# Optimization experiments

Hardware: AMD Instinct MI355X
Metric: run time of the kernel (lower is better)

The kernel has to match this reference:

```python
import jax, jax.numpy as jnp
import numpy as np

B, T, DIM = 4, 2048, 512
HEADS, HD = 8, 64
RANK = 256
WIN = 256
EPS = 1e-6
ROPE_BASE = 10000.0


def _rope_tables(seq_len, head_dim):
    pos = jnp.arange(seq_len, dtype=jnp.float32)                      # [T]
    inv_freq = 1.0 / (ROPE_BASE ** (jnp.arange(0, head_dim, 2, dtype=jnp.float32) / head_dim))  # [HD/2]
    ang = pos[:, None] * inv_freq[None, :]                            # [T, HD/2]
    cos = jnp.concatenate([jnp.cos(ang), jnp.cos(ang)], axis=-1)      # [T, HD]
    sin = jnp.concatenate([jnp.sin(ang), jnp.sin(ang)], axis=-1)
    return cos, sin


def _rotate_half(x):
    x1, x2 = jnp.split(x, 2, axis=-1)
    return jnp.concatenate([-x2, x1], axis=-1)


def _apply_rope(q, k):
    # q, k: [B, H, T, HD]
    cos, sin = _rope_tables(q.shape[2], q.shape[3])
    cos = cos[None, None]; sin = sin[None, None]
    q = q * cos + _rotate_half(q) * sin
    k = k * cos + _rotate_half(k) * sin
    return q, k


def _rmsnorm(x, w):
    x32 = x.astype(jnp.float32)
    n = x32 * jax.lax.rsqrt(jnp.mean(x32 * x32, axis=-1, keepdims=True) + EPS)
    return n.astype(x.dtype) * w


def setup_inputs() -> dict:
    key = jax.random.key(0)
    ks = jax.random.split(key, 6)
    s = 0.02
    return {
        "x": jax.random.normal(ks[0], (B, T, DIM), dtype=jnp.float32),
        "Wq": jax.random.normal(ks[1], (DIM, DIM), dtype=jnp.float32) * s,
        "Wkv_down": jax.random.normal(ks[2], (RANK, DIM), dtype=jnp.float32) * s,
        "kv_norm_w": jnp.ones((RANK,), dtype=jnp.float32),
        "Wkv_up": jax.random.normal(ks[3], (2 * DIM, RANK), dtype=jnp.float32) * s,
        "Wout": jax.random.normal(ks[4], (DIM, DIM), dtype=jnp.float32) * s,
    }


def reference(x, Wq, Wkv_down, kv_norm_w, Wkv_up, Wout):
    # q projection -> [B, H, T, HD]
    q = jnp.einsum('btd,ed->bte', x, Wq).reshape(B, T, HEADS, HD).transpose(0, 2, 1, 3)
    # latent KV: down-proj -> RMSNorm -> up-proj
    c_kv = jnp.einsum('btd,rd->btr', x, Wkv_down)          # [B, T, RANK]
    c_kv = _rmsnorm(c_kv, kv_norm_w)
    kv = jnp.einsum('btr,er->bte', c_kv, Wkv_up)            # [B, T, 2*DIM]
    kv = kv.reshape(B, T, 2, HEADS, HD).transpose(2, 0, 3, 1, 4)
    k, v = kv[0], kv[1]                                     # [B, H, T, HD]
    q, k = _apply_rope(q, k)
    rows = jnp.arange(T)[:, None]
    cols = jnp.arange(T)[None, :]
    mask = jnp.abs(cols - rows) <= WIN                      # [T, T]
    scale = HD ** -0.5
    scores = jnp.einsum('bhtd,bhsd->bhts', q, k) * scale    # [B, H, T, T]
    scores = jnp.where(mask[None, None], scores, jnp.float32(-jnp.inf))
    attn = jax.nn.softmax(scores, axis=-1)
    out = jnp.einsum('bhts,bhsd->bhtd', attn, v)            # [B, H, T, HD]
    out = out.transpose(0, 2, 1, 3).reshape(B, T, DIM)
    return jnp.einsum('btd,ed->bte', out, Wout)
```

## Files before the change

kernel.cpp:

```cpp
#include <hip/hip_runtime.h>
#include <math.h>

#define BB 4
#define TT 2048
#define DIMM 512
#define HEADS 8
#define HDIM 64
#define RANKK 256
#define WINN 256

static constexpr int BT = BB * TT;
#define SC2 0.1803368801111244f

typedef short bf8_t __attribute__((ext_vector_type(8)));
typedef float f32x4 __attribute__((ext_vector_type(4)));

__device__ __forceinline__ unsigned short f2bf(float f) {
    unsigned u = __float_as_uint(f);
    u += 0x7fffu + ((u >> 16) & 1u);
    return (unsigned short)(u >> 16);
}
__device__ __forceinline__ unsigned f2bf2(float a, float b) {
    unsigned r;
    asm("v_cvt_pk_bf16_f32 %0, %1, %2" : "=v"(r) : "v"(a), "v"(b));
    return r;
}

typedef __attribute__((address_space(1))) void gvoid_t;
typedef __attribute__((address_space(3))) void lvoid_t;
__device__ __forceinline__ void gload16(const void* g, void* l) {
    __builtin_amdgcn_global_load_lds((gvoid_t*)g, (lvoid_t*)l, 16, 0, 0);
}
#define WAIT_VM0_BARRIER() do { \
    asm volatile("s_waitcnt vmcnt(0)" ::: "memory"); \
    __builtin_amdgcn_s_barrier(); \
    __builtin_amdgcn_sched_barrier(0); \
} while (0)

__device__ __forceinline__ void cvt4(const float* __restrict__ s,
                                     unsigned short* __restrict__ d, int i) {
    float4 v = *reinterpret_cast<const float4*>(s + i);
    uint2 st = make_uint2(f2bf2(v.x, v.y), f2bf2(v.z, v.w));
    *reinterpret_cast<uint2*>(d + i) = st;
}

__global__ __launch_bounds__(256) void prep_kernel(
    const float* __restrict__ x, const float* __restrict__ Wq,
    const float* __restrict__ Wkd, const float* __restrict__ Wku,
    const float* __restrict__ wn, const float* __restrict__ Wout,
    unsigned short* __restrict__ xb, unsigned short* __restrict__ wcomb,
    unsigned short* __restrict__ wkub, unsigned short* __restrict__ woutb,
    float* __restrict__ cosT, float* __restrict__ sinT) {
    int bid = blockIdx.x;
    if (bid < 4096) {
        cvt4(x, xb, (bid * 256 + threadIdx.x) * 4);
    } else if (bid < 4352) {
        cvt4(Wq, wcomb, ((bid - 4096) * 256 + threadIdx.x) * 4);
    } else if (bid < 4480) {
        cvt4(Wkd, wcomb + DIMM * DIMM, ((bid - 4352) * 256 + threadIdx.x) * 4);
    } else if (bid < 4736) {
        int i = ((bid - 4480) * 256 + threadIdx.x) * 4;
        float4 v = *reinterpret_cast<const float4*>(Wku + i);
        float4 s = *reinterpret_cast<const float4*>(wn + (i & 255));
        uint2 st = make_uint2(f2bf2(v.x * s.x, v.y * s.y), f2bf2(v.z * s.z, v.w * s.w));
        *reinterpret_cast<uint2*>(wkub + i) = st;
    } else if (bid < 4992) {
        cvt4(Wout, woutb, ((bid - 4736) * 256 + threadIdx.x) * 4);
    } else {
        int idx = (bid - 4992) * 256 + threadIdx.x;
        int t = idx >> 5, f = idx & 31;
        double freq = pow(10000.0, -(double)f / 32.0);
        double ang = (double)t * freq;
        cosT[idx] = (float)cos(ang);
        sinT[idx] = (float)sin(ang);
    }
}

template<int MODE, int BM>
__global__ __launch_bounds__(BM * 4) void gemm_bf(const unsigned short* __restrict__ A,
                                                  const unsigned short* __restrict__ W,
                                                  float* __restrict__ Cf,
                                                  unsigned short* __restrict__ O1,
                                                  unsigned short* __restrict__ O2,
                                                  const float* __restrict__ cosT,
                                                  const float* __restrict__ sinT,
                                                  float* __restrict__ ssum,
                                                  int K, int N) {
    __shared__ __align__(16) unsigned short As[2][BM * 64];
    __shared__ __align__(16) unsigned short Ws[2][128 * 64];
    const int tid = threadIdx.x;
    const int lane = tid & 63, w = tid >> 6;
    const int lr = lane & 15, hi = lane >> 4;
    const int m0 = blockIdx.x * BM, n0 = blockIdx.y * 128;
    const int wr = (w >> 1) * 32, wc = (w & 1) * 64;

    f32x4 acc[2][4];
#pragma unroll
    for (int i = 0; i < 2; ++i)
#pragma unroll
        for (int j = 0; j < 4; ++j) acc[i][j] = 0.0f;

    const int NT = K >> 6;
    auto stage = [&](int t, int b) {
        const int kt = t * 64;
#pragma unroll
        for (int c = tid; c < BM * 8; c += BM * 4) {
            int row = c >> 3, sc = ((c & 7) ^ (row & 7)) << 3;
            gload16(A + (size_t)(m0 + row) * K + kt + sc, &As[b][c * 8]);
        }
#pragma unroll
        for (int c = tid; c < 1024; c += BM * 4) {
            int row = c >> 3, sc = ((c & 7) ^ (row & 7)) << 3;
            gload16(W + (size_t)(n0 + row) * K + kt + sc, &Ws[b][c * 8]);
        }
    };

    stage(0, 0);
    WAIT_VM0_BARRIER();
    for (int t = 0; t < NT; ++t) {
        const int cur = t & 1;
        if (t + 1 < NT) stage(t + 1, cur ^ 1);
        bf8_t af[2][2], bw[4][2];
#pragma unroll
        for (int i = 0; i < 2; ++i) {
            int row = wr + i * 16 + lr;
#pragma unroll
            for (int kk = 0; kk < 2; ++kk)
                af[i][kk] = *reinterpret_cast<const bf8_t*>(
                    &As[cur][row * 64 + (((kk * 4 + hi) ^ (row & 7)) << 3)]);
        }
#pragma unroll
        for (int j = 0; j < 4; ++j) {
            int row = wc + j * 16 + lr;
#pragma unroll
            for (int kk = 0; kk < 2; ++kk)
                bw[j][kk] = *reinterpret_cast<const bf8_t*>(
                    &Ws[cur][row * 64 + (((kk * 4 + hi) ^ (row & 7)) << 3)]);
        }
#pragma unroll
        for (int kk = 0; kk < 2; ++kk)
#pragma unroll
            for (int i = 0; i < 2; ++i)
#pragma unroll
                for (int j = 0; j < 4; ++j)
                    acc[i][j] = __builtin_amdgcn_mfma_f32_16x16x32_bf16(af[i][kk], bw[j][kk], acc[i][j], 0, 0, 0);
        if (t + 1 < NT) WAIT_VM0_BARRIER();
    }

    if constexpr (MODE == 0) {
#pragma unroll
        for (int i = 0; i < 2; ++i)
#pragma unroll
            for (int j = 0; j < 4; ++j)
#pragma unroll
                for (int r = 0; r < 4; ++r)
                    Cf[(size_t)(m0 + wr + i * 16 + 4 * hi + r) * N + n0 + wc + j * 16 + lr] = acc[i][j][r];
    } else if (n0 < 512) {
        int h = (n0 + wc) >> 6;
#pragma unroll
        for (int i = 0; i < 2; ++i) {
            int tb = m0 + wr + i * 16 + 4 * hi;
            float4 rv4 = make_float4(1.f, 1.f, 1.f, 1.f);
            if constexpr (MODE == 2) {
                float4 sa = *reinterpret_cast<const float4*>(ssum + tb);
                float4 sb = *reinterpret_cast<const float4*>(ssum + 8192 + tb);
                float4 sc = *reinterpret_cast<const float4*>(ssum + 16384 + tb);
                float4 sd = *reinterpret_cast<const float4*>(ssum + 24576 + tb);
                rv4.x = rsqrtf((sa.x + sb.x + sc.x + sd.x) * (1.0f / RANKK) + 1e-6f);
                rv4.y = rsqrtf((sa.y + sb.y + sc.y + sd.y) * (1.0f / RANKK) + 1e-6f);
                rv4.z = rsqrtf((sa.z + sb.z + sc.z + sd.z) * (1.0f / RANKK) + 1e-6f);
                rv4.w = rsqrtf((sa.w + sb.w + sc.w + sd.w) * (1.0f / RANKK) + 1e-6f);
            }
#pragma unroll
            for (int j = 0; j < 2; ++j)
#pragma unroll
                for (int r = 0; r < 4; ++r) {
                    int t = tb + r;
                    int b = t >> 11, tt = t & 2047;
                    int ff = j * 16 + lr;
                    float rv = (&rv4.x)[r];
                    float x1 = acc[i][j][r] * rv, x2 = acc[i][j + 2][r] * rv;
                    float cc = cosT[tt * 32 + ff], ss = sinT[tt * 32 + ff];
                    unsigned u = f2bf2(x1 * cc - x2 * ss, x2 * cc + x1 * ss);
                    unsigned short* dp = O1 + ((size_t)((b * 8 + h) * 2048 + tt)) * 64;
                    dp[ff]      = (unsigned short)u;
                    dp[ff + 32] = (unsigned short)(u >> 16);
                }
        }
    } else if constexpr (MODE == 1) {
        int cb = n0 - 512 + wc;
        int part = ((n0 - 512) >> 7) * 2 + (w & 1);
#pragma unroll
        for (int i = 0; i < 2; ++i) {
            int tb = m0 + wr + i * 16 + 4 * hi;
#pragma unroll
            for (int r = 0; r < 4; ++r) {
                float ps = acc[i][0][r] * acc[i][0][r] + acc[i][1][r] * acc[i][1][r]
                         + acc[i][2][r] * acc[i][2][r] + acc[i][3][r] * acc[i][3][r];
                ps += __shfl_xor(ps, 1);
                ps += __shfl_xor(ps, 2);
                ps += __shfl_xor(ps, 4);
                ps += __shfl_xor(ps, 8);
                if (lr == 0) ssum[part * 8192 + tb + r] = ps;
            }
#pragma unroll
            for (int j = 0; j < 4; ++j) {
                unsigned a01 = f2bf2(acc[i][j][0], acc[i][j][1]);
                unsigned a23 = f2bf2(acc[i][j][2], acc[i][j][3]);
                unsigned short* dp = O2 + (size_t)tb * 256 + cb + j * 16 + lr;
                dp[0]   = (unsigned short)a01;
                dp[256] = (unsigned short)(a01 >> 16);
                dp[512] = (unsigned short)a23;
                dp[768] = (unsigned short)(a23 >> 16);
            }
        }
    } else {
        int cb = n0 + wc - 512;
        int h = cb >> 6;
#pragma unroll
        for (int i = 0; i < 2; ++i) {
            int tb = m0 + wr + i * 16 + 4 * hi;
            int b = tb >> 11, tt = tb & 2047;
            float4 sa = *reinterpret_cast<const float4*>(ssum + tb);
            float4 sb = *reinterpret_cast<const float4*>(ssum + 8192 + tb);
            float4 sc = *reinterpret_cast<const float4*>(ssum + 16384 + tb);
            float4 sd = *reinterpret_cast<const float4*>(ssum + 24576 + tb);
            float4 rv4;
            rv4.x = rsqrtf((sa.x + sb.x + sc.x + sd.x) * (1.0f / RANKK) + 1e-6f);
            rv4.y = rsqrtf((sa.y + sb.y + sc.y + sd.y) * (1.0f / RANKK) + 1e-6f);
            rv4.z = rsqrtf((sa.z + sb.z + sc.z + sd.z) * (1.0f / RANKK) + 1e-6f);
            rv4.w = rsqrtf((sa.w + sb.w + sc.w + sd.w) * (1.0f / RANKK) + 1e-6f);
#pragma unroll
            for (int j = 0; j < 4; ++j) {
                int hd = j * 16 + lr;
                uint2 st = make_uint2(f2bf2(acc[i][j][0] * rv4.x, acc[i][j][1] * rv4.y),
                                      f2bf2(acc[i][j][2] * rv4.z, acc[i][j][3] * rv4.w));
                *reinterpret_cast<uint2*>(O2 + (((size_t)(b * 8 + h) * 64 + hd) * 2048 + tt)) = st;
            }
        }
    }
}

__global__ __launch_bounds__(256) void attn_mfma(const unsigned short* __restrict__ qbf,
                                                 const unsigned short* __restrict__ kbf,
                                                 const unsigned short* __restrict__ vT,
                                                 unsigned short* __restrict__ aob) {
    __shared__ __align__(16) unsigned short Kl[2][64 * 64];
    __shared__ __align__(16) unsigned short Vl[2][64 * 64];
    __shared__ unsigned short Pl[128][72];
    const int tid = threadIdx.x;
    const int lane = tid & 63, w = tid >> 6;
    const int lr = lane & 15, hi = lane >> 4;

    const int fid = blockIdx.x;
    const int swz = (fid & 7) * 64 + (fid >> 3);
    const int t0 = (swz & 15) * 128;
    const int bh = swz >> 4;

    bf8_t qa[2][2];
#pragma unroll
    for (int qr = 0; qr < 2; ++qr) {
        const unsigned short* qp = qbf + ((size_t)bh * TT + t0 + w * 32 + qr * 16 + lr) * HDIM;
        qa[qr][0] = *reinterpret_cast<const bf8_t*>(qp + hi * 8);
        qa[qr][1] = *reinterpret_cast<const bf8_t*>(qp + 32 + hi * 8);
    }

    f32x4 oc[2][4];
#pragma unroll
    for (int qr = 0; qr < 2; ++qr)
#pragma unroll
        for (int f = 0; f < 4; ++f) oc[qr][f] = 0.0f;
    float lp[2][4] = {{0.f, 0.f, 0.f, 0.f}, {0.f, 0.f, 0.f, 0.f}};

    const int smin = max(0, t0 - WINN);
    const int smax = min(TT, t0 + 128 + WINN);
    const int NT = (smax - smin) >> 6;

    auto stage = [&](int t, int b) {
        const int s0 = smin + t * 64;
        int c0 = tid, c1 = tid + 256;
        int row0 = c0 >> 3, sc0 = ((c0 & 7) ^ (row0 & 7)) << 3;
        int row1 = c1 >> 3, sc1 = ((c1 & 7) ^ (row1 & 7)) << 3;
        gload16(kbf + ((size_t)bh * TT + s0 + row0) * HDIM + sc0, &Kl[b][c0 * 8]);
        gload16(kbf + ((size_t)bh * TT + s0 + row1) * HDIM + sc1, &Kl[b][c1 * 8]);
        gload16(vT + ((size_t)bh * 64 + row0) * TT + s0 + sc0, &Vl[b][c0 * 8]);
        gload16(vT + ((size_t)bh * 64 + row1) * TT + s0 + sc1, &Vl[b][c1 * 8]);
    };

    stage(0, 0);
    WAIT_VM0_BARRIER();
    for (int t = 0; t < NT; ++t) {
        const int cur = t & 1;
        if (t + 1 < NT) stage(t + 1, cur ^ 1);
        const int s0 = smin + t * 64;

        f32x4 sacc[2][4];
#pragma unroll
        for (int qr = 0; qr < 2; ++qr)
#pragma unroll
            for (int f = 0; f < 4; ++f) sacc[qr][f] = 0.0f;
        __builtin_amdgcn_s_setprio(1);
#pragma unroll
        for (int ks = 0; ks < 2; ++ks)
#pragma unroll
            for (int f = 0; f < 4; ++f) {
                int row = f * 16 + lr;
                bf8_t kb = *reinterpret_cast<const bf8_t*>(
                    &Kl[cur][row * 64 + (((ks * 4 + hi) ^ (row & 7)) << 3)]);
#pragma unroll
                for (int qr = 0; qr < 2; ++qr)
                    sacc[qr][f] = __builtin_amdgcn_mfma_f32_16x16x32_bf16(qa[qr][ks], kb, sacc[qr][f], 0, 0, 0);
            }
        __builtin_amdgcn_s_setprio(0);

        const int off_w = s0 - t0 - w * 32;
        const bool edge = (off_w + 63 > WINN) || (off_w - 31 < -WINN);
#pragma unroll
        for (int qr = 0; qr < 2; ++qr)
#pragma unroll
            for (int f = 0; f < 4; ++f) {
                float p[4];
#pragma unroll
                for (int r = 0; r < 4; ++r) {
                    float v;
                    if (edge) {
                        int d = off_w + f * 16 + lr - qr * 16 - 4 * hi - r;
                        v = (d <= WINN && d >= -WINN) ? exp2f(sacc[qr][f][r] * SC2) : 0.f;
                    } else {
                        v = exp2f(sacc[qr][f][r] * SC2);
                    }
                    p[r] = v;
                    lp[qr][r] += v;
                }
                unsigned a01 = f2bf2(p[0], p[1]);
                unsigned a23 = f2bf2(p[2], p[3]);
                unsigned short* bp = &Pl[w * 32 + qr * 16 + 4 * hi][f * 16 + lr];
                bp[0]   = (unsigned short)a01;
                bp[72]  = (unsigned short)(a01 >> 16);
                bp[144] = (unsigned short)a23;
                bp[216] = (unsigned short)(a23 >> 16);
            }

        __builtin_amdgcn_s_setprio(1);
#pragma unroll
        for (int ks = 0; ks < 2; ++ks) {
            bf8_t pa[2];
#pragma unroll
            for (int qr = 0; qr < 2; ++qr)
                pa[qr] = *reinterpret_cast<const bf8_t*>(&Pl[w * 32 + qr * 16 + lr][ks * 32 + hi * 8]);
#pragma unroll
            for (int f = 0; f < 4; ++f) {
                int row = f * 16 + lr;
                bf8_t vb = *reinterpret_cast<const bf8_t*>(
                    &Vl[cur][row * 64 + (((ks * 4 + hi) ^ (row & 7)) << 3)]);
#pragma unroll
                for (int qr = 0; qr < 2; ++qr)
                    oc[qr][f] = __builtin_amdgcn_mfma_f32_16x16x32_bf16(pa[qr], vb, oc[qr][f], 0, 0, 0);
            }
        }
        __builtin_amdgcn_s_setprio(0);
        if (t + 1 < NT) WAIT_VM0_BARRIER();
    }

#pragma unroll
    for (int qr = 0; qr < 2; ++qr)
#pragma unroll
        for (int r = 0; r < 4; ++r) {
            lp[qr][r] += __shfl_xor(lp[qr][r], 1);
            lp[qr][r] += __shfl_xor(lp[qr][r], 2);
            lp[qr][r] += __shfl_xor(lp[qr][r], 4);
            lp[qr][r] += __shfl_xor(lp[qr][r], 8);
        }

    int b = bh >> 3, h = bh & 7;
#pragma unroll
    for (int qr = 0; qr < 2; ++qr)
#pragma unroll
        for (int r = 0; r < 4; ++r) {
            float inv = 1.0f / lp[qr][r];
            int t = t0 + w * 32 + qr * 16 + 4 * hi + r;
            unsigned short* op = aob + ((size_t)b * TT + t) * DIMM + h * HDIM;
            unsigned u0 = f2bf2(oc[qr][0][r] * inv, oc[qr][1][r] * inv);
            unsigned u1 = f2bf2(oc[qr][2][r] * inv, oc[qr][3][r] * inv);
            op[lr]      = (unsigned short)u0;
            op[16 + lr] = (unsigned short)(u0 >> 16);
            op[32 + lr] = (unsigned short)u1;
            op[48 + lr] = (unsigned short)(u1 >> 16);
        }
}

extern "C" void kernel_launch(void* const* d_in, const int* in_sizes, int n_in,
                              void* d_out, int out_size, void* d_ws, size_t ws_size,
                              hipStream_t stream) {
    const float* x     = (const float*)d_in[0];
    const float* Wq    = (const float*)d_in[1];
    const float* Wkd   = (const float*)d_in[2];
    const float* wnorm = (const float*)d_in[3];
    const float* Wku   = (const float*)d_in[4];
    const float* Wout  = (const float*)d_in[5];
    float* out = (float*)d_out;
    char* ws = (char*)d_ws;

    unsigned short* xb    = (unsigned short*)(ws + 0);
    unsigned short* qb    = (unsigned short*)(ws + 8388608);
    unsigned short* kb    = (unsigned short*)(ws + 16777216);
    unsigned short* vTb   = (unsigned short*)(ws + 25165824);
    unsigned short* ckvb0 = (unsigned short*)(ws + 33554432);
    unsigned short* aob   = (unsigned short*)(ws + 37748736);
    unsigned short* wcomb = (unsigned short*)(ws + 46137344);
    unsigned short* wkub  = (unsigned short*)(ws + 46923776);
    unsigned short* woutb = (unsigned short*)(ws + 47448064);
    float*          cosT  = (float*)(ws + 48005120);
    float*          sinT  = (float*)(ws + 48267264);
    float*          ssum  = (float*)(ws + 48529408);

    prep_kernel<<<5248, 256, 0, stream>>>(x, Wq, Wkd, Wku, wnorm, Wout,
                                          xb, wcomb, wkub, woutb, cosT, sinT);

    gemm_bf<1, 64><<<dim3(BT / 64, 6), 256, 0, stream>>>(xb, wcomb, nullptr, qb, ckvb0,
                                                         cosT, sinT, ssum, DIMM, 768);

    gemm_bf<2, 128><<<dim3(BT / 128, 8), 512, 0, stream>>>(ckvb0, wkub, nullptr, kb, vTb,
                                                           cosT, sinT, ssum, RANKK, 1024);

    attn_mfma<<<512, 256, 0, stream>>>(qb, kb, vTb, aob);

    gemm_bf<0, 64><<<dim3(BT / 64, 4), 256, 0, stream>>>(aob, woutb, out, nullptr, nullptr,
                                                         nullptr, nullptr, nullptr, DIMM, DIMM);
}
```

Before: 81.19 us.

## Enlarge attention query tile to 256 rows with per-wave tile skipping, retile QKV GEMM

```diff
diff --git a/kernel.cpp b/kernel.cpp
--- a/kernel.cpp
+++ b/kernel.cpp
@@ -15,11 +15,6 @@
 typedef short bf8_t __attribute__((ext_vector_type(8)));
 typedef float f32x4 __attribute__((ext_vector_type(4)));
 
-__device__ __forceinline__ unsigned short f2bf(float f) {
-    unsigned u = __float_as_uint(f);
-    u += 0x7fffu + ((u >> 16) & 1u);
-    return (unsigned short)(u >> 16);
-}
 __device__ __forceinline__ unsigned f2bf2(float a, float b) {
     unsigned r;
     asm("v_cvt_pk_bf16_f32 %0, %1, %2" : "=v"(r) : "v"(a), "v"(b));
@@ -69,10 +64,11 @@
     } else {
         int idx = (bid - 4992) * 256 + threadIdx.x;
         int t = idx >> 5, f = idx & 31;
-        double freq = pow(10000.0, -(double)f / 32.0);
-        double ang = (double)t * freq;
-        cosT[idx] = (float)cos(ang);
-        sinT[idx] = (float)sin(ang);
+        double frev = exp2(-(double)f * 0.4152410118609203) * 0.15915494309189535;
+        double a = (double)t * frev;
+        float fr = (float)(a - floor(a));
+        cosT[idx] = cospif(2.0f * fr);
+        sinT[idx] = sinpif(2.0f * fr);
     }
 }
 
@@ -241,26 +237,27 @@
     }
 }
 
-__global__ __launch_bounds__(256) void attn_mfma(const unsigned short* __restrict__ qbf,
+__global__ __launch_bounds__(512) void attn_mfma(const unsigned short* __restrict__ qbf,
                                                  const unsigned short* __restrict__ kbf,
                                                  const unsigned short* __restrict__ vT,
                                                  unsigned short* __restrict__ aob) {
     __shared__ __align__(16) unsigned short Kl[2][64 * 64];
     __shared__ __align__(16) unsigned short Vl[2][64 * 64];
-    __shared__ unsigned short Pl[128][72];
+    __shared__ unsigned short Pl[256][72];
     const int tid = threadIdx.x;
     const int lane = tid & 63, w = tid >> 6;
     const int lr = lane & 15, hi = lane >> 4;
 
     const int fid = blockIdx.x;
-    const int swz = (fid & 7) * 64 + (fid >> 3);
-    const int t0 = (swz & 15) * 128;
-    const int bh = swz >> 4;
+    const int swz = (fid & 7) * 32 + (fid >> 3);
+    const int t0 = (swz & 7) * 256;
+    const int bh = swz >> 3;
+    const int wq0 = w * 32;
 
     bf8_t qa[2][2];
 #pragma unroll
     for (int qr = 0; qr < 2; ++qr) {
-        const unsigned short* qp = qbf + ((size_t)bh * TT + t0 + w * 32 + qr * 16 + lr) * HDIM;
+        const unsigned short* qp = qbf + ((size_t)bh * TT + t0 + wq0 + qr * 16 + lr) * HDIM;
         qa[qr][0] = *reinterpret_cast<const bf8_t*>(qp + hi * 8);
         qa[qr][1] = *reinterpret_cast<const bf8_t*>(qp + 32 + hi * 8);
     }
@@ -273,18 +270,16 @@
     float lp[2][4] = {{0.f, 0.f, 0.f, 0.f}, {0.f, 0.f, 0.f, 0.f}};
 
     const int smin = max(0, t0 - WINN);
-    const int smax = min(TT, t0 + 128 + WINN);
+    const int smax = min(TT, t0 + 256 + WINN);
     const int NT = (smax - smin) >> 6;
+
+    const int st_row = tid >> 3;
+    const int st_cs = ((tid & 7) ^ (st_row & 7)) << 3;
 
     auto stage = [&](int t, int b) {
         const int s0 = smin + t * 64;
-        int c0 = tid, c1 = tid + 256;
-        int row0 = c0 >> 3, sc0 = ((c0 & 7) ^ (row0 & 7)) << 3;
-        int row1 = c1 >> 3, sc1 = ((c1 & 7) ^ (row1 & 7)) << 3;
-        gload16(kbf + ((size_t)bh * TT + s0 + row0) * HDIM + sc0, &Kl[b][c0 * 8]);
-        gload16(kbf + ((size_t)bh * TT + s0 + row1) * HDIM + sc1, &Kl[b][c1 * 8]);
-        gload16(vT + ((size_t)bh * 64 + row0) * TT + s0 + sc0, &Vl[b][c0 * 8]);
-        gload16(vT + ((size_t)bh * 64 + row1) * TT + s0 + sc1, &Vl[b][c1 * 8]);
+        gload16(kbf + ((size_t)bh * TT + s0 + st_row) * HDIM + st_cs, &Kl[b][tid * 8]);
+        gload16(vT + ((size_t)bh * 64 + st_row) * TT + s0 + st_cs, &Vl[b][tid * 8]);
     };
 
     stage(0, 0);
@@ -293,72 +288,75 @@
         const int cur = t & 1;
         if (t + 1 < NT) stage(t + 1, cur ^ 1);
         const int s0 = smin + t * 64;
-
-        f32x4 sacc[2][4];
-#pragma unroll
-        for (int qr = 0; qr < 2; ++qr)
-#pragma unroll
-            for (int f = 0; f < 4; ++f) sacc[qr][f] = 0.0f;
-        __builtin_amdgcn_s_setprio(1);
-#pragma unroll
-        for (int ks = 0; ks < 2; ++ks)
-#pragma unroll
-            for (int f = 0; f < 4; ++f) {
-                int row = f * 16 + lr;
-                bf8_t kb = *reinterpret_cast<const bf8_t*>(
-                    &Kl[cur][row * 64 + (((ks * 4 + hi) ^ (row & 7)) << 3)]);
+        const int off_w = s0 - t0 - wq0;
+        const bool active = (off_w >= -(WINN + 63)) && (off_w <= WINN + 31);
+
+        if (active) {
+            f32x4 sacc[2][4];
+#pragma unroll
+            for (int qr = 0; qr < 2; ++qr)
+#pragma unroll
+                for (int f = 0; f < 4; ++f) sacc[qr][f] = 0.0f;
+            __builtin_amdgcn_s_setprio(1);
+#pragma unroll
+            for (int ks = 0; ks < 2; ++ks)
+#pragma unroll
+                for (int f = 0; f < 4; ++f) {
+                    int row = f * 16 + lr;
+                    bf8_t kb = *reinterpret_cast<const bf8_t*>(
+                        &Kl[cur][row * 64 + (((ks * 4 + hi) ^ (row & 7)) << 3)]);
+#pragma unroll
+                    for (int qr = 0; qr < 2; ++qr)
+                        sacc[qr][f] = __builtin_amdgcn_mfma_f32_16x16x32_bf16(qa[qr][ks], kb, sacc[qr][f], 0, 0, 0);
+                }
+            __builtin_amdgcn_s_setprio(0);
+
+            const bool edge = (off_w + 63 > WINN) || (off_w - 31 < -WINN);
+#pragma unroll
+            for (int qr = 0; qr < 2; ++qr)
+#pragma unroll
+                for (int f = 0; f < 4; ++f) {
+                    float p[4];
+#pragma unroll
+                    for (int r = 0; r < 4; ++r) {
+                        float v;
+                        if (edge) {
+                            int d = off_w + f * 16 + lr - qr * 16 - 4 * hi - r;
+                            v = (d <= WINN && d >= -WINN) ? exp2f(sacc[qr][f][r] * SC2) : 0.f;
+                        } else {
+                            v = exp2f(sacc[qr][f][r] * SC2);
+                        }
+                        p[r] = v;
+                        lp[qr][r] += v;
+                    }
+                    unsigned a01 = f2bf2(p[0], p[1]);
+                    unsigned a23 = f2bf2(p[2], p[3]);
+                    unsigned short* bp = &Pl[wq0 + qr * 16 + 4 * hi][f * 16 + lr];
+                    bp[0]   = (unsigned short)a01;
+                    bp[72]  = (unsigned short)(a01 >> 16);
+                    bp[144] = (unsigned short)a23;
+                    bp[216] = (unsigned short)(a23 >> 16);
+                }
+
+            __builtin_amdgcn_s_setprio(1);
+#pragma unroll
+            for (int ks = 0; ks < 2; ++ks) {
+                bf8_t pa[2];
 #pragma unroll
                 for (int qr = 0; qr < 2; ++qr)
-                    sacc[qr][f] = __builtin_amdgcn_mfma_f32_16x16x32_bf16(qa[qr][ks], kb, sacc[qr][f], 0, 0, 0);
+                    pa[qr] = *reinterpret_cast<const bf8_t*>(&Pl[wq0 + qr * 16 + lr][ks * 32 + hi * 8]);
+#pragma unroll
+                for (int f = 0; f < 4; ++f) {
+                    int row = f * 16 + lr;
+                    bf8_t vb = *reinterpret_cast<const bf8_t*>(
+                        &Vl[cur][row * 64 + (((ks * 4 + hi) ^ (row & 7)) << 3)]);
+#pragma unroll
+                    for (int qr = 0; qr < 2; ++qr)
+                        oc[qr][f] = __builtin_amdgcn_mfma_f32_16x16x32_bf16(pa[qr], vb, oc[qr][f], 0, 0, 0);
+                }
             }
-        __builtin_amdgcn_s_setprio(0);
-
-        const int off_w = s0 - t0 - w * 32;
-        const bool edge = (off_w + 63 > WINN) || (off_w - 31 < -WINN);
-#pragma unroll
-        for (int qr = 0; qr < 2; ++qr)
-#pragma unroll
-            for (int f = 0; f < 4; ++f) {
-                float p[4];
-#pragma unroll
-                for (int r = 0; r < 4; ++r) {
-                    float v;
-                    if (edge) {
-                        int d = off_w + f * 16 + lr - qr * 16 - 4 * hi - r;
-                        v = (d <= WINN && d >= -WINN) ? exp2f(sacc[qr][f][r] * SC2) : 0.f;
-                    } else {
-                        v = exp2f(sacc[qr][f][r] * SC2);
-                    }
-                    p[r] = v;
-                    lp[qr][r] += v;
-                }
-                unsigned a01 = f2bf2(p[0], p[1]);
-                unsigned a23 = f2bf2(p[2], p[3]);
-                unsigned short* bp = &Pl[w * 32 + qr * 16 + 4 * hi][f * 16 + lr];
-                bp[0]   = (unsigned short)a01;
-                bp[72]  = (unsigned short)(a01 >> 16);
-                bp[144] = (unsigned short)a23;
-                bp[216] = (unsigned short)(a23 >> 16);
-            }
-
-        __builtin_amdgcn_s_setprio(1);
-#pragma unroll
-        for (int ks = 0; ks < 2; ++ks) {
-            bf8_t pa[2];
-#pragma unroll
-            for (int qr = 0; qr < 2; ++qr)
-                pa[qr] = *reinterpret_cast<const bf8_t*>(&Pl[w * 32 + qr * 16 + lr][ks * 32 + hi * 8]);
-#pragma unroll
-            for (int f = 0; f < 4; ++f) {
-                int row = f * 16 + lr;
-                bf8_t vb = *reinterpret_cast<const bf8_t*>(
-                    &Vl[cur][row * 64 + (((ks * 4 + hi) ^ (row & 7)) << 3)]);
-#pragma unroll
-                for (int qr = 0; qr < 2; ++qr)
-                    oc[qr][f] = __builtin_amdgcn_mfma_f32_16x16x32_bf16(pa[qr], vb, oc[qr][f], 0, 0, 0);
-            }
-        }
-        __builtin_amdgcn_s_setprio(0);
+            __builtin_amdgcn_s_setprio(0);
+        }
         if (t + 1 < NT) WAIT_VM0_BARRIER();
     }
 
@@ -378,7 +376,7 @@
 #pragma unroll
         for (int r = 0; r < 4; ++r) {
             float inv = 1.0f / lp[qr][r];
-            int t = t0 + w * 32 + qr * 16 + 4 * hi + r;
+            int t = t0 + wq0 + qr * 16 + 4 * hi + r;
             unsigned short* op = aob + ((size_t)b * TT + t) * DIMM + h * HDIM;
             unsigned u0 = f2bf2(oc[qr][0][r] * inv, oc[qr][1][r] * inv);
             unsigned u1 = f2bf2(oc[qr][2][r] * inv, oc[qr][3][r] * inv);
@@ -417,13 +415,13 @@
     prep_kernel<<<5248, 256, 0, stream>>>(x, Wq, Wkd, Wku, wnorm, Wout,
                                           xb, wcomb, wkub, woutb, cosT, sinT);
 
-    gemm_bf<1, 64><<<dim3(BT / 64, 6), 256, 0, stream>>>(xb, wcomb, nullptr, qb, ckvb0,
-                                                         cosT, sinT, ssum, DIMM, 768);
+    gemm_bf<1, 128><<<dim3(BT / 128, 6), 512, 0, stream>>>(xb, wcomb, nullptr, qb, ckvb0,
+                                                           cosT, sinT, ssum, DIMM, 768);
 
     gemm_bf<2, 128><<<dim3(BT / 128, 8), 512, 0, stream>>>(ckvb0, wkub, nullptr, kb, vTb,
                                                            cosT, sinT, ssum, RANKK, 1024);
 
-    attn_mfma<<<512, 256, 0, stream>>>(qb, kb, vTb, aob);
+    attn_mfma<<<256, 512, 0, stream>>>(qb, kb, vTb, aob);
 
     gemm_bf<0, 64><<<dim3(BT / 64, 4), 256, 0, stream>>>(aob, woutb, out, nullptr, nullptr,
                                                          nullptr, nullptr, nullptr, DIMM, DIMM);
```

Measured after the change: 83.28 us. +2.6%, slower.
